# Kernel tuning notes

Measured on AMD Instinct MI355X. Metric: run time of the kernel, lower is better.

Reference implementation:

```python
import jax, jax.numpy as jnp
import numpy as np

TD_DENOM = 3600.0  # td_upper - td_lower
SD_DENOM = 1000.0  # sd_upper - sd_lower

B, T, E, H = 64, 256, 512, 512
V, NB = 50000, 128


def setup_inputs() -> dict:
    key = jax.random.key(0)
    ks = jax.random.split(key, 16)
    s = 0.02
    return {
        'loc_seq': jax.random.randint(ks[0], (B, T), 0, V),
        'td_upper_seq': jax.random.randint(ks[1], (B, T), 0, NB),
        'td_lower_seq': jax.random.randint(ks[2], (B, T), 0, NB),
        'sd_upper_seq': jax.random.randint(ks[3], (B, T), 0, NB),
        'sd_lower_seq': jax.random.randint(ks[4], (B, T), 0, NB),
        'valid_lengths': jax.random.randint(ks[5], (B,), 1, T + 1),
        'loc_emb': jax.random.normal(ks[6], (V, E), jnp.float32) * s,
        't_up_emb': jax.random.normal(ks[7], (NB, E), jnp.float32) * s,
        't_lo_emb': jax.random.normal(ks[8], (NB, E), jnp.float32) * s,
        's_up_emb': jax.random.normal(ks[9], (NB, E), jnp.float32) * s,
        's_lo_emb': jax.random.normal(ks[10], (NB, E), jnp.float32) * s,
        'Wt': jax.random.normal(ks[11], (E, 3 * H), jnp.float32) * s,
        'Ws': jax.random.normal(ks[12], (E, 3 * H), jnp.float32) * s,
        'Wi': jax.random.normal(ks[13], (E, 4 * H), jnp.float32) * s,
        'bi': jnp.zeros((4 * H,), jnp.float32),
        'Wh': jax.random.normal(ks[14], (H, 4 * H), jnp.float32) * s,
    }


def reference(loc_seq, td_upper_seq, td_lower_seq, sd_upper_seq, sd_lower_seq,
              valid_lengths, loc_emb, t_up_emb, t_lo_emb, s_up_emb, s_lo_emb,
              Wt, Ws, Wi, bi, Wh):
    Bs, Ts = loc_seq.shape
    Hs = Wh.shape[0]
    x = loc_emb[loc_seq]                                            # (B,T,E)
    q = (t_up_emb[td_upper_seq] + t_lo_emb[td_lower_seq]) / TD_DENOM
    sp = (s_up_emb[sd_upper_seq] + s_lo_emb[sd_lower_seq]) / SD_DENOM
    # first_step zeroes q and s
    mask = (jnp.arange(Ts) > 0).astype(x.dtype)[None, :, None]
    q = q * mask
    sp = sp * mask
    Fp = jnp.einsum('bte,ef->btf', q, Wt) + jnp.einsum('bte,ef->btf', sp, Ws)  # (B,T,3H)
    xp = jnp.einsum('bte,ef->btf', x, Wi) + bi                                  # (B,T,4H)

    def step(carry, xs):
        h, c = carry
        xpt, Ft = xs
        tmp = xpt + h @ Wh
        i_t, f_t, o_t, g_t = jnp.split(tmp, 4, axis=1)
        i_F, f_F, o_F = jnp.split(Ft, 3, axis=1)
        i_t = jax.nn.sigmoid(i_t + i_F)
        f_t = jax.nn.sigmoid(f_t + f_F)
        o_t = jax.nn.sigmoid(o_t + o_F)
        g_t = jnp.tanh(g_t)
        c = f_t * c + i_t * g_t
        h = o_t * jnp.tanh(c)
        return (h, c), (h, c)

    h0 = jnp.zeros((Bs, Hs), x.dtype)
    c0 = jnp.zeros((Bs, Hs), x.dtype)
    (hT, cT), (hs, cs) = jax.lax.scan(
        step, (h0, c0), (xp.transpose(1, 0, 2), Fp.transpose(1, 0, 2)))
    all_h = hs.transpose(1, 0, 2)  # (B,T,H)
    all_c = cs.transpose(1, 0, 2)
    # original prepends the final hidden, then selects index (valid_length+1)-1
    all_h_full = jnp.concatenate([hT[:, None], all_h], axis=1)  # (B,T+1,H)
    all_c_full = jnp.concatenate([cT[:, None], all_c], axis=1)
    b_idx = jnp.arange(Bs)
    last_h = all_h_full[b_idx, valid_lengths]
    last_c = all_c_full[b_idx, valid_lengths]
    return (all_h, last_h, last_c)
```

## Files before the change

kernel.cpp:

```cpp
#include <hip/hip_runtime.h>
#include <stdint.h>

#define A_CAT_OFF  0ull
#define WCT_OFF    50331648ull
#define WHR_OFF    56623104ull
#define G_OFF      58720256ull
#define HBUF_OFF   125829120ull
#define DIST_OFF   126091264ull
#define WS_NEED    126091520ull

typedef short bf16x8 __attribute__((ext_vector_type(8)));
typedef float f32x4  __attribute__((ext_vector_type(4)));
typedef uint32_t u32x4 __attribute__((ext_vector_type(4)));

__device__ __forceinline__ unsigned short f2bf(float f) {
  union { float f; uint32_t u; } v; v.f = f;
  uint32_t u = v.u;
  u += 0x7FFFu + ((u >> 16) & 1u);
  return (unsigned short)(u >> 16);
}
__device__ __forceinline__ float bf2f(unsigned short h) {
  union { uint32_t u; float f; } v; v.u = ((uint32_t)h) << 16;
  return v.f;
}
__device__ __forceinline__ float u2f(uint32_t u) {
  union { uint32_t u; float f; } v; v.u = u; return v.f;
}
__device__ __forceinline__ uint32_t f2u(float f) {
  union { float f; uint32_t u; } v; v.f = f; return v.u;
}
__device__ __forceinline__ float fsigmoid(float x) { return 1.0f / (1.0f + __expf(-x)); }
__device__ __forceinline__ float ftanh(float x) {
  float e = __expf(2.0f * x);
  return 1.0f - 2.0f / (e + 1.0f);
}
__device__ __forceinline__ uint4 pack8(const unsigned short* v) {
  uint4 r;
  r.x = (uint32_t)v[0] | ((uint32_t)v[1] << 16);
  r.y = (uint32_t)v[2] | ((uint32_t)v[3] << 16);
  r.z = (uint32_t)v[4] | ((uint32_t)v[5] << 16);
  r.w = (uint32_t)v[6] | ((uint32_t)v[7] << 16);
  return r;
}
__device__ __forceinline__ uint32_t pk2(uint32_t a, uint32_t b) {
  return (uint32_t)f2bf(u2f(a)) | ((uint32_t)f2bf(u2f(b)) << 16);
}

#define GLOAD_LDS16(GP, LP)                                                   \
  __builtin_amdgcn_global_load_lds(                                          \
      (const __attribute__((address_space(1))) uint32_t*)(GP),               \
      (__attribute__((address_space(3))) uint32_t*)(LP), 16, 0, 0)

#define BAR_LDS()                                                             \
  do {                                                                        \
    asm volatile("s_waitcnt lgkmcnt(0)" ::: "memory");                        \
    __builtin_amdgcn_sched_barrier(0);                                        \
    __builtin_amdgcn_s_barrier();                                             \
  } while (0)

__global__ __launch_bounds__(256) void k_prep(
    const float* __restrict__ Wi, const float* __restrict__ Wt,
    const float* __restrict__ Ws, const float* __restrict__ Wh,
    uint8_t* ws) {
  int id = blockIdx.x * 256 + threadIdx.x;
  if (id < 393216) {
    int n  = id & 2047;
    int k0 = (id >> 11) << 3;
    unsigned short v[8];
#pragma unroll
    for (int j = 0; j < 8; ++j) {
      int k = k0 + j;
      float x;
      if (k < 512)       x = Wi[k * 2048 + n];
      else if (k < 1024) x = (n < 1536) ? Wt[(k - 512) * 1536 + n] : 0.0f;
      else               x = (n < 1536) ? Ws[(k - 1024) * 1536 + n] : 0.0f;
      v[j] = f2bf(x);
    }
    size_t off = WCT_OFF + (size_t)n * 3072 +
                 (size_t)(((uint32_t)k0 * 2u) ^ (((uint32_t)n & 7u) << 4));
    *(uint4*)(ws + off) = pack8(v);
  } else if (id < 524288) {
    int id2 = id - 393216;
    int cc  = id2 & 2047;
    int k0  = (id2 >> 11) << 3;
    int col = ((cc >> 5) & 3) * 512 + (cc >> 7) * 32 + (cc & 31);
    unsigned short v[8];
#pragma unroll
    for (int j = 0; j < 8; ++j) v[j] = f2bf(Wh[(size_t)(k0 + j) * 2048 + col]);
    *(uint4*)(ws + WHR_OFF + (size_t)cc * 1024 + (size_t)k0 * 2) = pack8(v);
  } else if (id < 532480) {
    uint4 z; z.x = z.y = z.z = z.w = 0u;
    *(uint4*)(ws + HBUF_OFF + (size_t)(id - 524288) * 16) = z;
  } else if (id < 540672) {
    uint4 z; z.x = z.y = z.z = z.w = 1u;
    *(uint4*)(ws + HBUF_OFF + 131072ull + (size_t)(id - 532480) * 16) = z;
  } else if (id < 540688) {
    uint4 z; z.x = z.y = z.z = z.w = 0u;
    *(uint4*)(ws + DIST_OFF + (size_t)(id - 540672) * 16) = z;
  }
}

__global__ __launch_bounds__(192) void k_gather(
    const int* __restrict__ loc, const int* __restrict__ tdu,
    const int* __restrict__ tdl, const int* __restrict__ sdu,
    const int* __restrict__ sdl,
    const float* __restrict__ loc_emb, const float* __restrict__ tup,
    const float* __restrict__ tlo, const float* __restrict__ sup,
    const float* __restrict__ slo, uint8_t* ws) {
  int m  = blockIdx.x;
  int t  = m & 255;
  int k0 = threadIdx.x << 3;
  float vals[8];
  if (k0 < 512) {
    const float* s = loc_emb + (size_t)loc[m] * 512 + k0;
#pragma unroll
    for (int j = 0; j < 8; ++j) vals[j] = s[j];
  } else if (k0 < 1024) {
    int e = k0 - 512;
    const float* a = tup + (size_t)tdu[m] * 512 + e;
    const float* b = tlo + (size_t)tdl[m] * 512 + e;
    float sc = (t > 0) ? (1.0f / 3600.0f) : 0.0f;
#pragma unroll
    for (int j = 0; j < 8; ++j) vals[j] = (a[j] + b[j]) * sc;
  } else {
    int e = k0 - 1024;
    const float* a = sup + (size_t)sdu[m] * 512 + e;
    const float* b = slo + (size_t)sdl[m] * 512 + e;
    float sc = (t > 0) ? (1.0f / 1000.0f) : 0.0f;
#pragma unroll
    for (int j = 0; j < 8; ++j) vals[j] = (a[j] + b[j]) * sc;
  }
  unsigned short v[8];
#pragma unroll
  for (int j = 0; j < 8; ++j) v[j] = f2bf(vals[j]);
  size_t off = A_CAT_OFF + (size_t)m * 3072 +
               (size_t)(((uint32_t)k0 * 2u) ^ (((uint32_t)m & 7u) << 4));
  *(uint4*)(ws + off) = pack8(v);
}

__global__ __launch_bounds__(256) void k_gemm(uint8_t* ws,
                                              const float* __restrict__ bi) {
  __shared__ uint8_t A_lds[16384];
  __shared__ uint8_t B_lds[16384];
  const uint8_t* Acat = ws + A_CAT_OFF;
  const uint8_t* Wct  = ws + WCT_OFF;
  uint8_t* Gp = ws + G_OFF;
  int tid = threadIdx.x;
  int lane = tid & 63, wave = tid >> 6;
  int wm = wave >> 1, wn = wave & 1;
  int tile_m = blockIdx.x >> 4, tile_n = blockIdx.x & 15;

  f32x4 acc[4][4];
#pragma unroll
  for (int m = 0; m < 4; ++m)
#pragma unroll
    for (int n = 0; n < 4; ++n) acc[m][n] = f32x4{0.f, 0.f, 0.f, 0.f};

  for (int kb = 0; kb < 1536; kb += 64) {
#pragma unroll
    for (int i = 0; i < 4; ++i) {
      int lidx = i * 256 + tid;
      int row = lidx >> 3, ch = lidx & 7;
      GLOAD_LDS16(Acat + (size_t)(tile_m * 128 + row) * 3072 + kb * 2 + ch * 16,
                  A_lds + (i * 256 + wave * 64) * 16);
    }
#pragma unroll
    for (int i = 0; i < 4; ++i) {
      int lidx = i * 256 + tid;
      int row = lidx >> 3, ch = lidx & 7;
      GLOAD_LDS16(Wct + (size_t)(tile_n * 128 + row) * 3072 + kb * 2 + ch * 16,
                  B_lds + (i * 256 + wave * 64) * 16);
    }
    __syncthreads();
#pragma unroll
    for (int kk = 0; kk < 2; ++kk) {
      int koff = kk * 64 + ((lane >> 4) << 4);
      bf16x8 af[4], bfr[4];
#pragma unroll
      for (int m = 0; m < 4; ++m) {
        int row = wm * 64 + m * 16 + (lane & 15);
        af[m] = *(const bf16x8*)(A_lds + row * 128 + (koff ^ ((row & 7) << 4)));
      }
#pragma unroll
      for (int n = 0; n < 4; ++n) {
        int row = wn * 64 + n * 16 + (lane & 15);
        bfr[n] = *(const bf16x8*)(B_lds + row * 128 + (koff ^ ((row & 7) << 4)));
      }
#pragma unroll
      for (int m = 0; m < 4; ++m)
#pragma unroll
        for (int n = 0; n < 4; ++n)
          acc[m][n] = __builtin_amdgcn_mfma_f32_16x16x32_bf16(af[m], bfr[n],
                                                              acc[m][n], 0, 0, 0);
    }
    __syncthreads();
  }
  int lr = lane >> 4, lc = lane & 15;
#pragma unroll
  for (int n = 0; n < 4; ++n) {
    int gcol = tile_n * 128 + wn * 64 + n * 16 + lc;
    float bv = bi[gcol];
    int gidx = (gcol & 511) * 4 + (gcol >> 9);
#pragma unroll
    for (int m = 0; m < 4; ++m) {
      int growb = tile_m * 128 + wm * 64 + m * 16 + lr * 4;
#pragma unroll
      for (int q = 0; q < 4; ++q) {
        int grow = growb + q;
        float v = acc[m][n][q] + bv;
        size_t gi = ((size_t)(grow & 255) * 64 + (size_t)(grow >> 8)) * 2048 + gidx;
        *(unsigned short*)(Gp + gi * 2) = f2bf(v);
      }
    }
  }
}

__global__ __launch_bounds__(576, 1) void k_recur(uint8_t* ws,
                                                  const int* __restrict__ vlen,
                                                  float* __restrict__ out) {
  int bid = blockIdx.x;
  if ((bid & 7) >= 4) return;
  int r = bid & 7, c = bid >> 3;

  extern __shared__ uint8_t smem[];
  uint8_t* h_lds   = smem;
  float*   tmp     = (float*)(smem + 16384);
  uint8_t* g_lds   = smem + 24832;
  float*   pub_lds = (float*)(smem + 33024);
  float*   c_lds   = (float*)(smem + 37120);

  int tid = threadIdx.x;
  int lane = tid & 63, wave = tid >> 6;

  const uint8_t* Gp = ws + G_OFF;
  uint8_t* hbuf = ws + HBUF_OFF;
  uint32_t* dist = (uint32_t*)(ws + DIST_OFF + (size_t)r * 64);

  float* outH  = out;
  float* outLH = out + 8388608;
  float* outLC = out + 8421376;

  bf16x8 Bfrag[16];
  int gb = tid >> 5, d = tid & 31;
  int gbatch = r * 16 + gb;
  int hb_b = 2 * wave + (lane >> 5);
  int w0 = lane & 31;
  float cr = 0.0f;
  uint32_t pubw_prev = 0;
  bool fb = false;

  int b8 = lane >> 2, seg = lane & 3;
  int w8b = r * 16 + b8;
  int w8vl = 0;
  uint4 gr0, gr1, gr2, gr3;

  if (wave < 8) {
    int cc = c * 128 + wave * 16 + (lane & 15);
    const uint8_t* wb = ws + WHR_OFF + (size_t)cc * 1024 + ((lane >> 4) << 4);
#pragma unroll
    for (int kk = 0; kk < 16; ++kk)
      Bfrag[kk] = *(const bf16x8*)(wb + kk * 64);
  } else {
    w8vl = vlen[w8b];
    const uint8_t* gp0 = Gp + (size_t)w8b * 4096 + (size_t)c * 256 + (size_t)seg * 64;
    uint4 a0 = *(const uint4*)(gp0);
    uint4 a1 = *(const uint4*)(gp0 + 16);
    uint4 a2 = *(const uint4*)(gp0 + 32);
    uint4 a3 = *(const uint4*)(gp0 + 48);
    uint8_t* gl = g_lds + b8 * 256 + seg * 64;
    *(uint4*)(gl)      = a0;
    *(uint4*)(gl + 16) = a1;
    *(uint4*)(gl + 32) = a2;
    *(uint4*)(gl + 48) = a3;
    const uint8_t* gp1 = gp0 + 262144;
    gr0 = *(const uint4*)(gp1);
    gr1 = *(const uint4*)(gp1 + 16);
    gr2 = *(const uint4*)(gp1 + 32);
    gr3 = *(const uint4*)(gp1 + 48);
  }

  __syncthreads();

  for (int t = 0; t < 256; ++t) {
    uint8_t* mybuf = hbuf + (size_t)(t & 1) * 131072;
    if (wave < 8) {
      uint32_t* mypub = (uint32_t*)(mybuf + (size_t)gbatch * 2048 +
                                    (size_t)(c * 32 + d) * 4);
      u32x4 x0, x1, x2, x3;
      {
        const uint8_t* hb = mybuf + (size_t)r * 32768 +
                            (size_t)hb_b * 2048 + (size_t)w0 * 64;
        uint32_t expect = (uint32_t)((t >> 1) & 1);
        int passes = 0;
        for (;;) {
          if (!fb) {
            asm volatile(
              "global_load_dwordx4 %0, %4, off sc0\n\t"
              "global_load_dwordx4 %1, %5, off sc0\n\t"
              "global_load_dwordx4 %2, %6, off sc0\n\t"
              "global_load_dwordx4 %3, %7, off sc0\n\t"
              "s_waitcnt vmcnt(0)"
              : "=v"(x0), "=v"(x1), "=v"(x2), "=v"(x3)
              : "v"(hb), "v"(hb + 16), "v"(hb + 32), "v"(hb + 48)
              : "memory");
            __builtin_amdgcn_sched_barrier(0);
          } else {
            uint64_t y[8];
#pragma unroll
            for (int i = 0; i < 8; ++i)
              y[i] = __hip_atomic_load((const uint64_t*)(hb + i * 8),
                                       __ATOMIC_RELAXED, __HIP_MEMORY_SCOPE_AGENT);
            x0 = u32x4{(uint32_t)y[0], (uint32_t)(y[0] >> 32), (uint32_t)y[1], (uint32_t)(y[1] >> 32)};
            x1 = u32x4{(uint32_t)y[2], (uint32_t)(y[2] >> 32), (uint32_t)y[3], (uint32_t)(y[3] >> 32)};
            x2 = u32x4{(uint32_t)y[4], (uint32_t)(y[4] >> 32), (uint32_t)y[5], (uint32_t)(y[5] >> 32)};
            x3 = u32x4{(uint32_t)y[6], (uint32_t)(y[6] >> 32), (uint32_t)y[7], (uint32_t)(y[7] >> 32)};
          }
          uint32_t bad = 0;
#pragma unroll
          for (int e = 0; e < 4; ++e)
            bad |= (x0[e] ^ expect) | (x1[e] ^ expect) |
                   (x2[e] ^ expect) | (x3[e] ^ expect);
          if (__ballot((bad & 1u) != 0u) == 0ULL) break;
          ++passes;
          if (passes == 64 && !fb) {
            uint32_t dv = __hip_atomic_load(dist, __ATOMIC_RELAXED,
                                            __HIP_MEMORY_SCOPE_AGENT);
            if (__ballot(dv != 0) != 0ULL) {
              fb = true;
              __hip_atomic_store(mypub, pubw_prev, __ATOMIC_RELAXED,
                                 __HIP_MEMORY_SCOPE_AGENT);
            }
          }
          if (passes > 1024) {
            passes = 512;
            if (!fb) {
              fb = true;
              __hip_atomic_store(dist, 1u, __ATOMIC_RELAXED,
                                 __HIP_MEMORY_SCOPE_AGENT);
            }
            __hip_atomic_store(mypub, pubw_prev, __ATOMIC_RELAXED,
                               __HIP_MEMORY_SCOPE_AGENT);
          }
        }
      }
      {
        uint4 v0, v1;
        v0.x = pk2(x0[0], x0[1]); v0.y = pk2(x0[2], x0[3]);
        v0.z = pk2(x1[0], x1[1]); v0.w = pk2(x1[2], x1[3]);
        v1.x = pk2(x2[0], x2[1]); v1.y = pk2(x2[2], x2[3]);
        v1.z = pk2(x3[0], x3[1]); v1.w = pk2(x3[2], x3[3]);
        int s = hb_b & 7;
        int c0 = (2 * w0) ^ (w0 >> 2) ^ s;
        int c1 = c0 ^ 1;
        *(uint4*)(h_lds + hb_b * 1024 + c0 * 16) = v0;
        *(uint4*)(h_lds + hb_b * 1024 + c1 * 16) = v1;
      }
    } else {
      asm volatile("s_waitcnt vmcnt(0)" ::: "memory");
      __builtin_amdgcn_sched_barrier(0);
      {
        uint8_t* gl = g_lds + ((t + 1) & 1) * 4096 + b8 * 256 + seg * 64;
        *(uint4*)(gl)      = gr0;
        *(uint4*)(gl + 16) = gr1;
        *(uint4*)(gl + 32) = gr2;
        *(uint4*)(gl + 48) = gr3;
      }
      if (t > 0) {
        const float* pl = pub_lds + ((t + 1) & 1) * 512 + b8 * 32 + seg * 8;
        float4 h0 = *(const float4*)pl;
        float4 h1 = *(const float4*)(pl + 4);
        float* oh = outH + ((size_t)w8b * 256 + (size_t)(t - 1)) * 512 +
                    (size_t)(c * 32 + seg * 8);
        *(float4*)oh = h0;
        *(float4*)(oh + 4) = h1;
        if (t - 1 == w8vl - 1) {
          const float* cl = c_lds + ((t + 1) & 1) * 512 + b8 * 32 + seg * 8;
          float4 cv0 = *(const float4*)cl;
          float4 cv1 = *(const float4*)(cl + 4);
          size_t lb = (size_t)w8b * 512 + (size_t)(c * 32 + seg * 8);
          *(float4*)(outLH + lb) = h0;
          *(float4*)(outLH + lb + 4) = h1;
          *(float4*)(outLC + lb) = cv0;
          *(float4*)(outLC + lb + 4) = cv1;
        }
      }
      {
        const uint8_t* gp = Gp + (size_t)(((t + 2) & 255) * 64 + w8b) * 4096 +
                            (size_t)c * 256 + (size_t)seg * 64;
        gr0 = *(const uint4*)(gp);
        gr1 = *(const uint4*)(gp + 16);
        gr2 = *(const uint4*)(gp + 32);
        gr3 = *(const uint4*)(gp + 48);
      }
    }
    BAR_LDS();

    if (wave < 8) {
      f32x4 acc0 = f32x4{0.f, 0.f, 0.f, 0.f}, acc1 = acc0;
      {
        int lrow = lane & 15;
        int g = lane >> 4;
        int gs = (g ^ (lrow & 7)) * 16;
#pragma unroll
        for (int kk = 0; kk < 16; kk += 2) {
          int k0c = ((kk * 4) ^ (kk >> 1)) * 16;
          int k1c = (((kk + 1) * 4) ^ ((kk + 1) >> 1)) * 16;
          bf16x8 a0 = *(const bf16x8*)(h_lds + lrow * 1024 + (k0c ^ gs));
          bf16x8 a1 = *(const bf16x8*)(h_lds + lrow * 1024 + (k1c ^ gs));
          acc0 = __builtin_amdgcn_mfma_f32_16x16x32_bf16(a0, Bfrag[kk], acc0, 0, 0, 0);
          acc1 = __builtin_amdgcn_mfma_f32_16x16x32_bf16(a1, Bfrag[kk + 1], acc1, 0, 0, 0);
        }
      }
      {
        int colb = wave * 16 + (lane & 15);
        int rowd = (lane >> 4) << 2;
#pragma unroll
        for (int q = 0; q < 4; ++q)
          tmp[(rowd + q) * 132 + colb] = acc0[q] + acc1[q];
      }
    }
    BAR_LDS();

    if (wave < 8) {
      float hval, cval;
      {
        uint64_t gx = *(const uint64_t*)(g_lds + (t & 1) * 4096 + gb * 256 + d * 8);
        int tb = gb * 132 + d;
        float ip = tmp[tb]      + bf2f((unsigned short)(gx & 0xFFFF));
        float fp = tmp[tb + 32] + bf2f((unsigned short)((gx >> 16) & 0xFFFF));
        float op = tmp[tb + 64] + bf2f((unsigned short)((gx >> 32) & 0xFFFF));
        float gp = tmp[tb + 96] + bf2f((unsigned short)((gx >> 48) & 0xFFFF));
        float ig = fsigmoid(ip), fg = fsigmoid(fp), og = fsigmoid(op);
        float gt = ftanh(gp);
        cval = fg * cr + ig * gt;
        cr = cval;
        hval = og * ftanh(cval);
      }
      {
        uint32_t wtag = (uint32_t)(((t + 1) >> 1) & 1);
        uint32_t pubw = (f2u(hval) & ~1u) | wtag;
        uint32_t* pub = (uint32_t*)(hbuf + (size_t)((t + 1) & 1) * 131072 +
                                    (size_t)gbatch * 2048 + (size_t)(c * 32 + d) * 4);
        asm volatile("global_store_dword %0, %1, off" :: "v"(pub), "v"(pubw) : "memory");
        if (fb)
          __hip_atomic_store(pub, pubw, __ATOMIC_RELAXED, __HIP_MEMORY_SCOPE_AGENT);
        asm volatile("s_waitcnt vmcnt(0)" ::: "memory");
        __builtin_amdgcn_sched_barrier(0);
        pubw_prev = pubw;
      }
      pub_lds[(t & 1) * 512 + tid] = hval;
      c_lds[(t & 1) * 512 + tid] = cval;
    }
    BAR_LDS();
  }
  if (wave == 8) {
    const float* pl = pub_lds + 512 + b8 * 32 + seg * 8;
    float4 h0 = *(const float4*)pl;
    float4 h1 = *(const float4*)(pl + 4);
    float* oh = outH + ((size_t)w8b * 256 + 255) * 512 + (size_t)(c * 32 + seg * 8);
    *(float4*)oh = h0;
    *(float4*)(oh + 4) = h1;
    if (w8vl == 256) {
      const float* cl = c_lds + 512 + b8 * 32 + seg * 8;
      float4 cv0 = *(const float4*)cl;
      float4 cv1 = *(const float4*)(cl + 4);
      size_t lb = (size_t)w8b * 512 + (size_t)(c * 32 + seg * 8);
      *(float4*)(outLH + lb) = h0;
      *(float4*)(outLH + lb + 4) = h1;
      *(float4*)(outLC + lb) = cv0;
      *(float4*)(outLC + lb + 4) = cv1;
    }
  }
}

extern "C" void kernel_launch(void* const* d_in, const int* in_sizes, int n_in,
                              void* d_out, int out_size, void* d_ws, size_t ws_size,
                              hipStream_t stream) {
  const int*   loc     = (const int*)d_in[0];
  const int*   tdu     = (const int*)d_in[1];
  const int*   tdl     = (const int*)d_in[2];
  const int*   sdu     = (const int*)d_in[3];
  const int*   sdl     = (const int*)d_in[4];
  const int*   vlen    = (const int*)d_in[5];
  const float* loc_emb = (const float*)d_in[6];
  const float* tup     = (const float*)d_in[7];
  const float* tlo     = (const float*)d_in[8];
  const float* sup     = (const float*)d_in[9];
  const float* slo     = (const float*)d_in[10];
  const float* Wt      = (const float*)d_in[11];
  const float* Ws      = (const float*)d_in[12];
  const float* Wi      = (const float*)d_in[13];
  const float* bi      = (const float*)d_in[14];
  const float* Wh      = (const float*)d_in[15];
  uint8_t* ws = (uint8_t*)d_ws;
  float* out = (float*)d_out;

  if (ws_size < WS_NEED) return;

  (void)hipFuncSetAttribute((const void*)k_recur,
                            hipFuncAttributeMaxDynamicSharedMemorySize, 98304);

  k_prep  <<<2113, 256, 0, stream>>>(Wi, Wt, Ws, Wh, ws);
  k_gather<<<16384, 192, 0, stream>>>(loc, tdu, tdl, sdu, sdl,
                                      loc_emb, tup, tlo, sup, slo, ws);
  k_gemm  <<<2048, 256, 0, stream>>>(ws, bi);
  k_recur <<<128, 576, 98304, stream>>>(ws, vlen, out);
}
```

Before: 1.369 ms.

## Replace per-element tag-bit polling with per-block step-counter sentinels

The cross-block handshake in the recurrent kernel changes. Before, every hidden value carried a phase tag in its low bit, and consumers polled the full 64-byte h slices. Now each block publishes a monotonically increasing step counter after its barrier, and consumers poll 16 counters with one dword per lane before loading h untagged. This cuts polling traffic and keeps full h precision, but it adds a second serial global round trip per step (sentinel first, then data), plus a sentinel store after the barrier. The fallback detection also moves to a periodic dist check shared through LDS.

Result: slower. 1.419 ms (+3.7%).

```diff
diff --git a/kernel.cpp b/kernel.cpp
--- a/kernel.cpp
+++ b/kernel.cpp
@@ -7,7 +7,8 @@
 #define G_OFF      58720256ull
 #define HBUF_OFF   125829120ull
 #define DIST_OFF   126091264ull
-#define WS_NEED    126091520ull
+#define SENT_OFF   126091520ull
+#define WS_NEED    126091776ull
 
 typedef short bf16x8 __attribute__((ext_vector_type(8)));
 typedef float f32x4  __attribute__((ext_vector_type(4)));
@@ -91,12 +92,9 @@
   } else if (id < 532480) {
     uint4 z; z.x = z.y = z.z = z.w = 0u;
     *(uint4*)(ws + HBUF_OFF + (size_t)(id - 524288) * 16) = z;
-  } else if (id < 540672) {
-    uint4 z; z.x = z.y = z.z = z.w = 1u;
-    *(uint4*)(ws + HBUF_OFF + 131072ull + (size_t)(id - 532480) * 16) = z;
-  } else if (id < 540688) {
+  } else if (id < 532512) {
     uint4 z; z.x = z.y = z.z = z.w = 0u;
-    *(uint4*)(ws + DIST_OFF + (size_t)(id - 540672) * 16) = z;
+    *(uint4*)(ws + DIST_OFF + (size_t)(id - 532480) * 16) = z;
   }
 }
 
@@ -228,13 +226,16 @@
   uint8_t* g_lds   = smem + 24832;
   float*   pub_lds = (float*)(smem + 33024);
   float*   c_lds   = (float*)(smem + 37120);
+  volatile uint32_t* fbl = (volatile uint32_t*)(smem + 41216);
 
   int tid = threadIdx.x;
   int lane = tid & 63, wave = tid >> 6;
+  if (tid == 0) fbl[0] = 0;
 
   const uint8_t* Gp = ws + G_OFF;
   uint8_t* hbuf = ws + HBUF_OFF;
   uint32_t* dist = (uint32_t*)(ws + DIST_OFF + (size_t)r * 64);
+  uint32_t* sent = (uint32_t*)(ws + SENT_OFF + (size_t)r * 64);
 
   float* outH  = out;
   float* outLH = out + 8388608;
@@ -246,8 +247,12 @@
   int hb_b = 2 * wave + (lane >> 5);
   int w0 = lane & 31;
   float cr = 0.0f;
-  uint32_t pubw_prev = 0;
   bool fb = false;
+  uint32_t ph0 = 0, ph1 = 0;
+  uint32_t sent_prev = 0;
+  uint32_t* pubA = (uint32_t*)(hbuf + (size_t)gbatch * 2048 + (size_t)(c * 32 + d) * 4);
+  uint32_t* pubB = (uint32_t*)((uint8_t*)pubA + 131072);
+  uint32_t* sent_self = sent + c;
 
   int b8 = lane >> 2, seg = lane & 3;
   int w8b = r * 16 + b8;
@@ -284,63 +289,70 @@
   for (int t = 0; t < 256; ++t) {
     uint8_t* mybuf = hbuf + (size_t)(t & 1) * 131072;
     if (wave < 8) {
-      uint32_t* mypub = (uint32_t*)(mybuf + (size_t)gbatch * 2048 +
-                                    (size_t)(c * 32 + d) * 4);
-      u32x4 x0, x1, x2, x3;
-      {
-        const uint8_t* hb = mybuf + (size_t)r * 32768 +
-                            (size_t)hb_b * 2048 + (size_t)w0 * 64;
-        uint32_t expect = (uint32_t)((t >> 1) & 1);
+      if (!fb && fbl[0] != 0) {
+        fb = true;
+        __hip_atomic_store(pubA, ph0, __ATOMIC_RELAXED, __HIP_MEMORY_SCOPE_AGENT);
+        __hip_atomic_store(pubB, ph1, __ATOMIC_RELAXED, __HIP_MEMORY_SCOPE_AGENT);
+        if (tid == 0)
+          __hip_atomic_store(sent_self, sent_prev, __ATOMIC_RELAXED,
+                             __HIP_MEMORY_SCOPE_AGENT);
+      }
+      {
+        const uint32_t* sp = sent + (lane & 15);
         int passes = 0;
         for (;;) {
+          uint32_t sv;
           if (!fb) {
-            asm volatile(
-              "global_load_dwordx4 %0, %4, off sc0\n\t"
-              "global_load_dwordx4 %1, %5, off sc0\n\t"
-              "global_load_dwordx4 %2, %6, off sc0\n\t"
-              "global_load_dwordx4 %3, %7, off sc0\n\t"
-              "s_waitcnt vmcnt(0)"
-              : "=v"(x0), "=v"(x1), "=v"(x2), "=v"(x3)
-              : "v"(hb), "v"(hb + 16), "v"(hb + 32), "v"(hb + 48)
-              : "memory");
+            asm volatile("global_load_dword %0, %1, off sc0\n\t"
+                         "s_waitcnt vmcnt(0)"
+                         : "=v"(sv) : "v"(sp) : "memory");
             __builtin_amdgcn_sched_barrier(0);
           } else {
-            uint64_t y[8];
-#pragma unroll
-            for (int i = 0; i < 8; ++i)
-              y[i] = __hip_atomic_load((const uint64_t*)(hb + i * 8),
-                                       __ATOMIC_RELAXED, __HIP_MEMORY_SCOPE_AGENT);
-            x0 = u32x4{(uint32_t)y[0], (uint32_t)(y[0] >> 32), (uint32_t)y[1], (uint32_t)(y[1] >> 32)};
-            x1 = u32x4{(uint32_t)y[2], (uint32_t)(y[2] >> 32), (uint32_t)y[3], (uint32_t)(y[3] >> 32)};
-            x2 = u32x4{(uint32_t)y[4], (uint32_t)(y[4] >> 32), (uint32_t)y[5], (uint32_t)(y[5] >> 32)};
-            x3 = u32x4{(uint32_t)y[6], (uint32_t)(y[6] >> 32), (uint32_t)y[7], (uint32_t)(y[7] >> 32)};
+            sv = __hip_atomic_load(sp, __ATOMIC_RELAXED, __HIP_MEMORY_SCOPE_AGENT);
           }
-          uint32_t bad = 0;
-#pragma unroll
-          for (int e = 0; e < 4; ++e)
-            bad |= (x0[e] ^ expect) | (x1[e] ^ expect) |
-                   (x2[e] ^ expect) | (x3[e] ^ expect);
-          if (__ballot((bad & 1u) != 0u) == 0ULL) break;
-          ++passes;
-          if (passes == 64 && !fb) {
-            uint32_t dv = __hip_atomic_load(dist, __ATOMIC_RELAXED,
-                                            __HIP_MEMORY_SCOPE_AGENT);
-            if (__ballot(dv != 0) != 0ULL) {
-              fb = true;
-              __hip_atomic_store(mypub, pubw_prev, __ATOMIC_RELAXED,
-                                 __HIP_MEMORY_SCOPE_AGENT);
-            }
-          }
-          if (passes > 1024) {
+          if (__ballot(sv < (uint32_t)t) == 0ULL) break;
+          if (++passes > 1024) {
             passes = 512;
             if (!fb) {
               fb = true;
-              __hip_atomic_store(dist, 1u, __ATOMIC_RELAXED,
-                                 __HIP_MEMORY_SCOPE_AGENT);
+              if (lane == 0)
+                __hip_atomic_store(dist, 1u, __ATOMIC_RELAXED,
+                                   __HIP_MEMORY_SCOPE_AGENT);
+              fbl[0] = 1;
+              __hip_atomic_store(pubA, ph0, __ATOMIC_RELAXED, __HIP_MEMORY_SCOPE_AGENT);
+              __hip_atomic_store(pubB, ph1, __ATOMIC_RELAXED, __HIP_MEMORY_SCOPE_AGENT);
+              if (tid == 0)
+                __hip_atomic_store(sent_self, sent_prev, __ATOMIC_RELAXED,
+                                   __HIP_MEMORY_SCOPE_AGENT);
             }
-            __hip_atomic_store(mypub, pubw_prev, __ATOMIC_RELAXED,
-                               __HIP_MEMORY_SCOPE_AGENT);
           }
+        }
+      }
+      u32x4 x0, x1, x2, x3;
+      {
+        const uint8_t* hb = mybuf + (size_t)r * 32768 +
+                            (size_t)hb_b * 2048 + (size_t)w0 * 64;
+        if (!fb) {
+          asm volatile(
+            "global_load_dwordx4 %0, %4, off sc0\n\t"
+            "global_load_dwordx4 %1, %5, off sc0\n\t"
+            "global_load_dwordx4 %2, %6, off sc0\n\t"
+            "global_load_dwordx4 %3, %7, off sc0\n\t"
+            "s_waitcnt vmcnt(0)"
+            : "=v"(x0), "=v"(x1), "=v"(x2), "=v"(x3)
+            : "v"(hb), "v"(hb + 16), "v"(hb + 32), "v"(hb + 48)
+            : "memory");
+          __builtin_amdgcn_sched_barrier(0);
+        } else {
+          uint64_t y[8];
+#pragma unroll
+          for (int i = 0; i < 8; ++i)
+            y[i] = __hip_atomic_load((const uint64_t*)(hb + i * 8),
+                                     __ATOMIC_RELAXED, __HIP_MEMORY_SCOPE_AGENT);
+          x0 = u32x4{(uint32_t)y[0], (uint32_t)(y[0] >> 32), (uint32_t)y[1], (uint32_t)(y[1] >> 32)};
+          x1 = u32x4{(uint32_t)y[2], (uint32_t)(y[2] >> 32), (uint32_t)y[3], (uint32_t)(y[3] >> 32)};
+          x2 = u32x4{(uint32_t)y[4], (uint32_t)(y[4] >> 32), (uint32_t)y[5], (uint32_t)(y[5] >> 32)};
+          x3 = u32x4{(uint32_t)y[6], (uint32_t)(y[6] >> 32), (uint32_t)y[7], (uint32_t)(y[7] >> 32)};
         }
       }
       {
@@ -392,6 +404,11 @@
         gr2 = *(const uint4*)(gp + 32);
         gr3 = *(const uint4*)(gp + 48);
       }
+      if ((t & 15) == 0 && lane == 0) {
+        uint32_t dv = __hip_atomic_load(dist, __ATOMIC_RELAXED,
+                                        __HIP_MEMORY_SCOPE_AGENT);
+        if (dv != 0) fbl[0] = 1;
+      }
     }
     BAR_LDS();
 
@@ -437,21 +454,26 @@
         hval = og * ftanh(cval);
       }
       {
-        uint32_t wtag = (uint32_t)(((t + 1) >> 1) & 1);
-        uint32_t pubw = (f2u(hval) & ~1u) | wtag;
-        uint32_t* pub = (uint32_t*)(hbuf + (size_t)((t + 1) & 1) * 131072 +
-                                    (size_t)gbatch * 2048 + (size_t)(c * 32 + d) * 4);
+        uint32_t pubw = f2u(hval);
+        uint32_t* pub = (((t + 1) & 1) == 0) ? pubA : pubB;
         asm volatile("global_store_dword %0, %1, off" :: "v"(pub), "v"(pubw) : "memory");
         if (fb)
           __hip_atomic_store(pub, pubw, __ATOMIC_RELAXED, __HIP_MEMORY_SCOPE_AGENT);
+        if (((t + 1) & 1) == 0) ph0 = pubw; else ph1 = pubw;
+        pub_lds[(t & 1) * 512 + tid] = hval;
+        c_lds[(t & 1) * 512 + tid] = cval;
         asm volatile("s_waitcnt vmcnt(0)" ::: "memory");
         __builtin_amdgcn_sched_barrier(0);
-        pubw_prev = pubw;
-      }
-      pub_lds[(t & 1) * 512 + tid] = hval;
-      c_lds[(t & 1) * 512 + tid] = cval;
+      }
     }
     BAR_LDS();
+    if (wave < 8 && tid == 0) {
+      uint32_t sval = (uint32_t)(t + 1);
+      asm volatile("global_store_dword %0, %1, off" :: "v"(sent_self), "v"(sval) : "memory");
+      if (fb)
+        __hip_atomic_store(sent_self, sval, __ATOMIC_RELAXED, __HIP_MEMORY_SCOPE_AGENT);
+      sent_prev = sval;
+    }
   }
   if (wave == 8) {
     const float* pl = pub_lds + 512 + b8 * 32 + seg * 8;
@@ -500,7 +522,7 @@
   (void)hipFuncSetAttribute((const void*)k_recur,
                             hipFuncAttributeMaxDynamicSharedMemorySize, 98304);
 
-  k_prep  <<<2113, 256, 0, stream>>>(Wi, Wt, Ws, Wh, ws);
+  k_prep  <<<2081, 256, 0, stream>>>(Wi, Wt, Ws, Wh, ws);
   k_gather<<<16384, 192, 0, stream>>>(loc, tdu, tdl, sdu, sdl,
                                       loc_emb, tup, tlo, sup, slo, ws);
   k_gemm  <<<2048, 256, 0, stream>>>(ws, bi);
```
